# Optimization experiments

Hardware: AMD Instinct MI355X
Metric: run time of the kernel (lower is better)

Reference implementation:

```python
import jax, jax.numpy as jnp
from jax import lax
import numpy as np

DIVISOR = 2.0

def setup_inputs() -> dict:
    key = jax.random.key(0)
    k1, k2, k3, k4 = jax.random.split(key, 4)
    B, Cin, D, H, W = 64, 8, 32, 64, 64
    Cout, KD, KH, KW = 16, 3, 3, 3
    fan_in = Cin * KD * KH * KW
    bound = 1.0 / np.sqrt(fan_in)
    x = jax.random.normal(k1, (B, Cin, D, H, W), dtype=jnp.float32)
    conv_weight = jax.random.uniform(k2, (Cout, Cin, KD, KH, KW), jnp.float32, -bound, bound)
    conv_bias = jax.random.uniform(k3, (Cout,), jnp.float32, -bound, bound)
    bias = jax.random.normal(k4, (Cout, 1, 1, 1), dtype=jnp.float32) * 0.02
    return {"x": x, "conv_weight": conv_weight, "conv_bias": conv_bias, "bias": bias}

def reference(x, conv_weight, conv_bias, bias):
    # Conv3d, stride 1, no padding, groups=1  -> [B, Cout, D-2, H-2, W-2]
    y = lax.conv_general_dilated(
        x, conv_weight, window_strides=(1, 1, 1), padding='VALID',
        dimension_numbers=('NCDHW', 'OIDHW', 'NCDHW'))
    y = y + conv_bias[None, :, None, None, None]
    # Divide by constant
    y = y / DIVISOR
    # MaxPool3d(kernel=2, stride=2), floor mode (VALID drops the trailing odd row)
    y = lax.reduce_window(y, -jnp.inf, lax.max,
                          window_dimensions=(1, 1, 2, 2, 2),
                          window_strides=(1, 1, 2, 2, 2), padding='VALID')
    # AdaptiveAvgPool3d((1,1,1)) == global mean over spatial dims
    y = jnp.mean(y, axis=(2, 3, 4), keepdims=True)  # [B, Cout, 1, 1, 1]
    # Bias add (broadcast over batch)
    y = y + bias[None]
    # Sum over channel dim (sum_dim=1, no keepdim)
    return jnp.sum(y, axis=1)  # [B, 1, 1, 1]
```

## Files before the change

kernel.cpp:

```cpp
#include <hip/hip_runtime.h>

typedef __attribute__((ext_vector_type(8))) short short8;
typedef __attribute__((ext_vector_type(4))) float f32x4;
typedef unsigned int u32;

#define ROW_B 1056
#define SLOT_B 10560
#define NSLOT 4
#define CSTRIDE 131072

__device__ __forceinline__ unsigned short f2bf(float f) {
  unsigned u = __builtin_bit_cast(unsigned, f);
  u += 0x7FFFu + ((u >> 16) & 1u);
  return (unsigned short)(u >> 16);
}
__device__ __forceinline__ u32 cvtpk(float lo, float hi) {
  u32 r;
  asm("v_cvt_pk_bf16_f32 %0, %1, %2" : "=v"(r) : "v"(lo), "v"(hi));
  return r;
}

#define MF(ACC, H, FR, KD, KH)                                                \
  ACC[H][wt] = __builtin_amdgcn_mfma_f32_16x16x32_bf16(FR, bfragB[KD][KH],    \
                                                       ACC[H][wt], 0, 0, 0)
#define MFI(ACC, H, FR)                                                       \
  ACC[H][wt] = __builtin_amdgcn_mfma_f32_16x16x32_bf16(FR, bfragB[0][0],      \
                                                       zf4, 0, 0, 0)

#define PROC(DP, AN, AM, AO, K0, K1, K2, DOCLOSE, SAVEP, DOSTAGE, DOBAR)      \
  {                                                                           \
    const int dp_ = (DP);                                                     \
    if (DOSTAGE) {                                                            \
      stage_load(dp_ + 2);                                                    \
      __builtin_amdgcn_sched_barrier(0);     \
    }                                                                         \
    const int sb_ = (dp_ & 3) * SLOT_B + rowbase;                             \
    __builtin_amdgcn_s_setprio(1);                                            \
    _Pragma("unroll") for (int wt = 0; wt < 4; ++wt) {                        \
      const short8 f0 = *(const short8*)(smem + sb_ + 0 * ROW_B + physoff[wt]); \
      const short8 f1 = *(const short8*)(smem + sb_ + 1 * ROW_B + physoff[wt]); \
      const short8 f2 = *(const short8*)(smem + sb_ + 2 * ROW_B + physoff[wt]); \
      const short8 f3 = *(const short8*)(smem + sb_ + 3 * ROW_B + physoff[wt]); \
      if (K0) {                                                               \
        MFI(AN, 0, f0); MFI(AN, 1, f1);                                       \
        MF(AN, 0, f1, 0, 1); MF(AN, 1, f2, 0, 1);                             \
        MF(AN, 0, f2, 0, 2); MF(AN, 1, f3, 0, 2);                             \
      }                                                                       \
      if (K1) {                                                               \
        MF(AM, 0, f0, 1, 0); MF(AM, 1, f1, 1, 0);                             \
        MF(AM, 0, f1, 1, 1); MF(AM, 1, f2, 1, 1);                             \
        MF(AM, 0, f2, 1, 2); MF(AM, 1, f3, 1, 2);                             \
      }                                                                       \
      if (K2) {                                                               \
        MF(AO, 0, f0, 2, 0); MF(AO, 1, f1, 2, 0);                             \
        MF(AO, 0, f1, 2, 1); MF(AO, 1, f2, 2, 1);                             \
        MF(AO, 0, f2, 2, 2); MF(AO, 1, f3, 2, 2);                             \
      }                                                                       \
    }                                                                         \
    __builtin_amdgcn_s_setprio(0);                                            \
    if (DOCLOSE) {                                                            \
      _Pragma("unroll") for (int wt = 0; wt < 4; ++wt) {                      \
        const float e01 = fmaxf(fmaxf(AO[0][wt][0], AO[0][wt][1]),            \
                                fmaxf(AO[1][wt][0], AO[1][wt][1]));           \
        const float e23 = fmaxf(fmaxf(AO[0][wt][2], AO[0][wt][3]),            \
                                fmaxf(AO[1][wt][2], AO[1][wt][3]));           \
        if (SAVEP) {                                                          \
          p01[wt] = e01; p23[wt] = e23;                                       \
        } else if (hvalid) {                                                  \
          sum += fmaxf(p01[wt], e01);                                         \
          if (!(wt == 3 && g == 3)) sum += fmaxf(p23[wt], e23);               \
        }                                                                     \
      }                                                                       \
    }                                                                         \
    if (DOSTAGE) stage_write(dp_ + 2);                                        \
    if (DOBAR) __syncthreads();                                               \
  }

__launch_bounds__(256, 2)
__global__ void conv_fused(const float* __restrict__ x,
                           const float* __restrict__ cw,
                           float* __restrict__ ws) {
  __shared__ __align__(16) unsigned char smem[NSLOT * SLOT_B];
  __shared__ float wsum[4];

  const int rb  = blockIdx.x;
  const int bid = (rb & 7) * 64 + (rb >> 3);
  const int b   = bid >> 3;
  const int hq  = bid & 7;
  const int h0  = hq * 8;

  const int tid  = threadIdx.x;
  const int lane = tid & 63;
  const int wid  = tid >> 6;
  const int nm   = lane & 15;
  const int g    = lane >> 4;

  const float* xb = x + (size_t)b * (8u * 32u * 64u * 64u);

  short8 bfragB[3][3];
#pragma unroll
  for (int kd = 0; kd < 3; ++kd)
#pragma unroll
    for (int kh = 0; kh < 3; ++kh) {
      short8 f;
#pragma unroll
      for (int j = 0; j < 8; ++j) {
        float v = (g < 3) ? cw[(nm * 8 + j) * 27 + kd * 9 + kh * 3 + g] : 0.f;
        f[j] = (short)f2bf(v);
      }
      bfragB[kd][kh] = f;
    }

  const int gc = (g < 3) ? g : 2;
  int physoff[4];
#pragma unroll
  for (int wt = 0; wt < 4; ++wt) physoff[wt] = (wt * 16 + nm + gc) * 16;
  const int rowbase = (2 * wid) * ROW_B;

  bool st_act[3]; int st_toff[3]; int st_off[3];
#pragma unroll
  for (int pass = 0; pass < 3; ++pass) {
    const int t = tid + pass * 256;
    bool act = (t < 640);
    int row = (t >> 6) % 10;
    const int w = t & 63;
    int h = h0 + row;
    if (h > 63) { act = false; h = 63; }
    st_act[pass]  = act;
    st_toff[pass] = h * 64 + w;
    st_off[pass]  = row * ROW_B + w * 16;
  }

  float ld[3][8];

  auto stage_load = [&](int p) {
    const int pbase = p * 4096;
#pragma unroll
    for (int pass = 0; pass < 3; ++pass) {
      if (st_act[pass]) {
        const int o = st_toff[pass] + pbase;
#pragma unroll
        for (int c = 0; c < 8; ++c)
          ld[pass][c] = (xb + (size_t)c * CSTRIDE)[o];
      }
    }
  };
  auto stage_write = [&](int p) {
    unsigned char* d = smem + (p & 3) * SLOT_B;
#pragma unroll
    for (int pass = 0; pass < 3; ++pass) {
      if (st_act[pass]) {
        uint4 v;
        v.x = cvtpk(ld[pass][0], ld[pass][1]);
        v.y = cvtpk(ld[pass][2], ld[pass][3]);
        v.z = cvtpk(ld[pass][4], ld[pass][5]);
        v.w = cvtpk(ld[pass][6], ld[pass][7]);
        *(uint4*)(d + st_off[pass]) = v;
      }
    }
  };

  const bool hvalid = !(hq == 7 && wid == 3);
  const f32x4 zf4 = {0.f, 0.f, 0.f, 0.f};
  float sum = 0.f;
  float p01[4], p23[4];
  f32x4 accA[2][4], accB[2][4], accC[2][4];

  stage_load(0); stage_write(0);
  stage_load(1); stage_write(1);
  __syncthreads();

  PROC(0, accA, accB, accC, 1, 0, 0, 0, 0, 1, 0)
  PROC(1, accB, accA, accC, 1, 1, 0, 0, 0, 1, 1)

  for (int p0 = 2; p0 <= 20; p0 += 6) {
    PROC(p0 + 0, accC, accB, accA, 1, 1, 1, 1, 1, 1, 0)
    PROC(p0 + 1, accA, accC, accB, 1, 1, 1, 1, 0, 1, 1)
    PROC(p0 + 2, accB, accA, accC, 1, 1, 1, 1, 1, 1, 0)
    PROC(p0 + 3, accC, accB, accA, 1, 1, 1, 1, 0, 1, 1)
    PROC(p0 + 4, accA, accC, accB, 1, 1, 1, 1, 1, 1, 0)
    PROC(p0 + 5, accB, accA, accC, 1, 1, 1, 1, 0, 1, 1)
  }
  PROC(26, accC, accB, accA, 1, 1, 1, 1, 1, 1, 0)
  PROC(27, accA, accC, accB, 1, 1, 1, 1, 0, 1, 1)
  PROC(28, accB, accA, accC, 1, 1, 1, 1, 1, 1, 0)
  PROC(29, accC, accB, accA, 1, 1, 1, 1, 0, 1, 1)
  PROC(30, accA, accC, accB, 0, 1, 1, 1, 1, 0, 0)
  PROC(31, accB, accA, accC, 0, 0, 1, 1, 0, 0, 0)

#pragma unroll
  for (int off = 32; off > 0; off >>= 1) sum += __shfl_down(sum, off);
  if (lane == 0) wsum[wid] = sum;
  __syncthreads();
  if (tid == 0) ws[bid] = wsum[0] + wsum[1] + wsum[2] + wsum[3];
}

__global__ void finalize_k(const float* __restrict__ ws,
                           const float* __restrict__ cb,
                           const float* __restrict__ bias,
                           float* __restrict__ out) {
  const int b = threadIdx.x;
  float s = 0.f;
#pragma unroll
  for (int hq = 0; hq < 8; ++hq) s += ws[b * 8 + hq];
  float cbs = 0.f, bs = 0.f;
#pragma unroll
  for (int c = 0; c < 16; ++c) { cbs += cb[c]; bs += bias[c]; }
  out[b] = 0.5f * s / 14415.f + 0.5f * cbs + bs;
}

extern "C" void kernel_launch(void* const* d_in, const int* in_sizes, int n_in,
                              void* d_out, int out_size, void* d_ws, size_t ws_size,
                              hipStream_t stream) {
  const float* x    = (const float*)d_in[0];
  const float* cw   = (const float*)d_in[1];
  const float* cb   = (const float*)d_in[2];
  const float* bias = (const float*)d_in[3];
  float* out = (float*)d_out;
  float* ws  = (float*)d_ws;

  hipLaunchKernelGGL(conv_fused, dim3(512), dim3(256), 0, stream, x, cw, ws);
  hipLaunchKernelGGL(finalize_k, dim3(1), dim3(64), 0, stream, ws, cb, bias, out);
}
```

Measured before the change: 77.38 us.

## Prefetch global loads one depth-plane ahead and use lightweight LDS barriers

Restructures the staging pipeline so global loads for plane p+3 are issued after the MFMA work of plane p. Their results are written to LDS in the following iteration, giving the loads a full iteration of latency hiding instead of being issued right before use. It also replaces __syncthreads with a barrier that waits only on LDS counters (lgkmcnt), so outstanding global loads are not drained at each barrier. In exchange, the loaded values stay live in registers across iterations, raising register pressure under the 2-blocks-per-CU launch bound.

New measurement: 78.90 us. No clear change (+2.0%).

```diff
diff --git a/kernel.cpp b/kernel.cpp
--- a/kernel.cpp
+++ b/kernel.cpp
@@ -19,6 +19,13 @@
   asm("v_cvt_pk_bf16_f32 %0, %1, %2" : "=v"(r) : "v"(lo), "v"(hi));
   return r;
 }
+
+#define LBAR()                                                                \
+  {                                                                           \
+    asm volatile("s_waitcnt lgkmcnt(0)" ::: "memory");                        \
+    __builtin_amdgcn_s_barrier();                                             \
+    __builtin_amdgcn_sched_barrier(0);                                        \
+  }
 
 #define MF(ACC, H, FR, KD, KH)                                                \
   ACC[H][wt] = __builtin_amdgcn_mfma_f32_16x16x32_bf16(FR, bfragB[KD][KH],    \
@@ -27,13 +34,9 @@
   ACC[H][wt] = __builtin_amdgcn_mfma_f32_16x16x32_bf16(FR, bfragB[0][0],      \
                                                        zf4, 0, 0, 0)
 
-#define PROC(DP, AN, AM, AO, K0, K1, K2, DOCLOSE, SAVEP, DOSTAGE, DOBAR)      \
+#define PROC(DP, AN, AM, AO, K0, K1, K2, DOCLOSE, SAVEP, WR, LDNEXT, DOBAR)   \
   {                                                                           \
     const int dp_ = (DP);                                                     \
-    if (DOSTAGE) {                                                            \
-      stage_load(dp_ + 2);                                                    \
-      __builtin_amdgcn_sched_barrier(0);     \
-    }                                                                         \
     const int sb_ = (dp_ & 3) * SLOT_B + rowbase;                             \
     __builtin_amdgcn_s_setprio(1);                                            \
     _Pragma("unroll") for (int wt = 0; wt < 4; ++wt) {                        \
@@ -58,6 +61,8 @@
       }                                                                       \
     }                                                                         \
     __builtin_amdgcn_s_setprio(0);                                            \
+    if (WR) stage_write(dp_ + 2);                                             \
+    if (LDNEXT) stage_load(dp_ + 3);                                          \
     if (DOCLOSE) {                                                            \
       _Pragma("unroll") for (int wt = 0; wt < 4; ++wt) {                      \
         const float e01 = fmaxf(fmaxf(AO[0][wt][0], AO[0][wt][1]),            \
@@ -72,8 +77,7 @@
         }                                                                     \
       }                                                                       \
     }                                                                         \
-    if (DOSTAGE) stage_write(dp_ + 2);                                        \
-    if (DOBAR) __syncthreads();                                               \
+    if (DOBAR) LBAR()                                                         \
   }
 
 __launch_bounds__(256, 2)
@@ -168,25 +172,26 @@
 
   stage_load(0); stage_write(0);
   stage_load(1); stage_write(1);
-  __syncthreads();
-
-  PROC(0, accA, accB, accC, 1, 0, 0, 0, 0, 1, 0)
-  PROC(1, accB, accA, accC, 1, 1, 0, 0, 0, 1, 1)
+  stage_load(2);
+  LBAR()
+
+  PROC(0, accA, accB, accC, 1, 0, 0, 0, 0, 1, 1, 0)
+  PROC(1, accB, accA, accC, 1, 1, 0, 0, 0, 1, 1, 1)
 
   for (int p0 = 2; p0 <= 20; p0 += 6) {
-    PROC(p0 + 0, accC, accB, accA, 1, 1, 1, 1, 1, 1, 0)
-    PROC(p0 + 1, accA, accC, accB, 1, 1, 1, 1, 0, 1, 1)
-    PROC(p0 + 2, accB, accA, accC, 1, 1, 1, 1, 1, 1, 0)
-    PROC(p0 + 3, accC, accB, accA, 1, 1, 1, 1, 0, 1, 1)
-    PROC(p0 + 4, accA, accC, accB, 1, 1, 1, 1, 1, 1, 0)
-    PROC(p0 + 5, accB, accA, accC, 1, 1, 1, 1, 0, 1, 1)
-  }
-  PROC(26, accC, accB, accA, 1, 1, 1, 1, 1, 1, 0)
-  PROC(27, accA, accC, accB, 1, 1, 1, 1, 0, 1, 1)
-  PROC(28, accB, accA, accC, 1, 1, 1, 1, 1, 1, 0)
-  PROC(29, accC, accB, accA, 1, 1, 1, 1, 0, 1, 1)
-  PROC(30, accA, accC, accB, 0, 1, 1, 1, 1, 0, 0)
-  PROC(31, accB, accA, accC, 0, 0, 1, 1, 0, 0, 0)
+    PROC(p0 + 0, accC, accB, accA, 1, 1, 1, 1, 1, 1, 1, 0)
+    PROC(p0 + 1, accA, accC, accB, 1, 1, 1, 1, 0, 1, 1, 1)
+    PROC(p0 + 2, accB, accA, accC, 1, 1, 1, 1, 1, 1, 1, 0)
+    PROC(p0 + 3, accC, accB, accA, 1, 1, 1, 1, 0, 1, 1, 1)
+    PROC(p0 + 4, accA, accC, accB, 1, 1, 1, 1, 1, 1, 1, 0)
+    PROC(p0 + 5, accB, accA, accC, 1, 1, 1, 1, 0, 1, 1, 1)
+  }
+  PROC(26, accC, accB, accA, 1, 1, 1, 1, 1, 1, 1, 0)
+  PROC(27, accA, accC, accB, 1, 1, 1, 1, 0, 1, 1, 1)
+  PROC(28, accB, accA, accC, 1, 1, 1, 1, 1, 1, 1, 0)
+  PROC(29, accC, accB, accA, 1, 1, 1, 1, 0, 1, 0, 1)
+  PROC(30, accA, accC, accB, 0, 1, 1, 1, 1, 0, 0, 0)
+  PROC(31, accB, accA, accC, 0, 0, 1, 1, 0, 0, 0, 0)
 
 #pragma unroll
   for (int off = 32; off > 0; off >>= 1) sum += __shfl_down(sum, off);
```
